# Kernel tuning notes

Measured on AMD Instinct MI355X. Metric: run time of the kernel, lower is better.

The kernel has to match this reference:

```python
import jax, jax.numpy as jnp
import numpy as np
from jax import lax

# db2 (Daubechies-2) filter bank, identical to pywt.Wavelet('db2')
_s3 = np.sqrt(3.0)
_dn = 4.0 * np.sqrt(2.0)
_h = np.array([(1 + _s3) / _dn, (3 + _s3) / _dn, (3 - _s3) / _dn, (1 - _s3) / _dn], dtype=np.float32)  # h0..h3
DEC_LO = jnp.asarray(_h[::-1].copy())                                                # [h3,h2,h1,h0]
DEC_HI = jnp.asarray(np.array([-_h[0], _h[1], -_h[2], _h[3]], dtype=np.float32))
REC_LO = jnp.asarray(_h)                                                             # [h0,h1,h2,h3]
REC_HI = jnp.asarray(np.array([_h[3], -_h[2], _h[1], -_h[0]], dtype=np.float32))
FL = 4  # filter length


def dwt1_symmetric(x):
    """pywt.wavedec level-1, mode='symmetric' along axis 1. x: [B,S,H] -> (cA,cD) each [B,(S+3)//2,H]."""
    B, S, H = x.shape
    M = (S + FL - 1) // 2
    xe = jnp.pad(x, ((0, 0), (FL - 1, FL - 1), (0, 0)), mode='symmetric')  # [B,S+6,H]

    def corr(w):
        # a[k] = sum_t w[FL-1-t] * xe[2k+1+t]
        return sum(w[FL - 1 - t] * xe[:, 1 + t:1 + t + 2 * M:2, :] for t in range(FL))

    return corr(DEC_LO), corr(DEC_HI)


def idwt1(ca, cd):
    """pywt.waverec level-1 (idwt). ca,cd: [B,Mc,H] -> [B,2*Mc-FL+2,H]."""
    B, Mc, H = ca.shape
    up_len = 2 * Mc - 1
    out_len = 2 * Mc - FL + 2

    def branch(c, f):
        u = jnp.zeros((B, up_len + 4, H), dtype=c.dtype)  # zero pad FL-2=2 each side
        u = u.at[:, 2:2 + up_len:2, :].set(c)             # upsample (zeros at odd positions)
        return sum(f[j] * u[:, 4 - j:4 - j + out_len, :] for j in range(FL))

    return branch(ca, REC_LO) + branch(cd, REC_HI)


def conv3_same(c, w, b):
    """torch Conv1d(H,H,3,padding=1) on channel-last c: [B,T,H]; w: [Hout,Hin,3], b: [Hout]."""
    y = lax.conv_general_dilated(c.transpose(0, 2, 1), w, window_strides=(1,),
                                 padding=((1, 1),), dimension_numbers=('NCH', 'OIH', 'NCH'))
    return (y + b[None, :, None]).transpose(0, 2, 1)


def setup_inputs() -> dict:
    key = jax.random.key(0)
    ks = jax.random.split(key, 7)
    B, S, H = 8, 2048, 1024
    sc_conv = 1.0 / np.sqrt(3 * H)
    sc_lin = 1.0 / np.sqrt(H)
    return {
        'x': jax.random.normal(ks[0], (B, S, H), jnp.float32),
        'w_approx': jax.random.normal(ks[1], (H, H, 3), jnp.float32) * sc_conv,
        'b_approx': jax.random.normal(ks[2], (H,), jnp.float32) * 0.01,
        'w_detail': jax.random.normal(ks[3], (H, H, 3), jnp.float32) * sc_conv,
        'b_detail': jax.random.normal(ks[4], (H,), jnp.float32) * 0.01,
        'w_out': jax.random.normal(ks[5], (H, H), jnp.float32) * sc_lin,
        'b_out': jax.random.normal(ks[6], (H,), jnp.float32) * 0.01,
    }


def reference(x, w_approx, b_approx, w_detail, b_detail, w_out, b_out):
    B, S, H = x.shape
    if S % 2 != 0:  # static pad to even length (matches torch code)
        x = jnp.pad(x, ((0, 0), (0, 1), (0, 0)))
        S += 1
    ca, cd = dwt1_symmetric(x)          # [B, S//2+1, H]
    target = S // 2
    ca, cd = ca[:, :target, :], cd[:, :target, :]  # truncate like the torch module
    pa = jax.nn.gelu(conv3_same(ca, w_approx, b_approx), approximate=False)
    pd = jax.nn.gelu(conv3_same(cd, w_detail, b_detail), approximate=False)
    recon = idwt1(pa, pd)               # [B, S-2, H]
    recon = jnp.pad(recon, ((0, 0), (0, S - recon.shape[1]), (0, 0)))  # zero-pad to S
    out = jnp.einsum('bsh,oh->bso', recon, w_out) + b_out  # output_proj; dropout=identity (eval)
    return out
```

## Files before the change

kernel.cpp:

```cpp
#include <hip/hip_runtime.h>
#include <hip/hip_bf16.h>
#include <math.h>


namespace {

constexpr int Hc = 1024;
constexpr int Sc = 2048;
constexpr int Mcv = 1024;
constexpr int AROWS = 1026;

constexpr double S3d = 1.7320508075688772935274463;
constexpr double DNd = 5.6568542494923801952067549;
constexpr float W0 = (float)((1.0 + S3d) / DNd);
constexpr float W1 = (float)((3.0 + S3d) / DNd);
constexpr float W2 = (float)((3.0 - S3d) / DNd);
constexpr float W3 = (float)((1.0 - S3d) / DNd);

typedef short bf16x8 __attribute__((ext_vector_type(8)));
typedef float f32x4 __attribute__((ext_vector_type(4)));

typedef __attribute__((address_space(1))) const unsigned char ga_u8;
typedef __attribute__((address_space(3))) unsigned char la_u8;

__device__ __forceinline__ void gload16(const void* g, void* l) {
  __builtin_amdgcn_global_load_lds((ga_u8*)g, (la_u8*)l, 16, 0, 0);
}

__device__ __forceinline__ unsigned short rnd1(float v) {
  __hip_bfloat16 hb = __float2bfloat16(v);
  return *reinterpret_cast<unsigned short*>(&hb);
}

__device__ __forceinline__ ushort4 rnd4(const float4 v) {
  ushort4 h;
  h.x = rnd1(v.x); h.y = rnd1(v.y); h.z = rnd1(v.z); h.w = rnd1(v.w);
  return h;
}

__device__ __forceinline__ void split1(float v, unsigned short& h, unsigned short& l) {
  __hip_bfloat16 hb = __float2bfloat16(v);
  float r = v - __bfloat162float(hb);
  __hip_bfloat16 lb = __float2bfloat16(r);
  h = *reinterpret_cast<unsigned short*>(&hb);
  l = *reinterpret_cast<unsigned short*>(&lb);
}

__device__ __forceinline__ void split4(const float4 v, ushort4& h, ushort4& l) {
  split1(v.x, h.x, l.x);
  split1(v.y, h.y, l.y);
  split1(v.z, h.z, l.z);
  split1(v.w, h.w, l.w);
}

__global__ void dwt_kernel(const float* __restrict__ x,
                           unsigned short* __restrict__ A) {
  const int tid = blockIdx.x * 256 + threadIdx.x;
  const int h4 = (tid & 255) << 2;
  const int m = (tid >> 8) & (Mcv - 1);
  const int b = tid >> 18;
  const float* xb = x + (size_t)b * Sc * Hc;
  float4 v[4];
#pragma unroll
  for (int t = 0; t < 4; ++t) {
    int i = 2 * m - 2 + t;
    if (i < 0) i = -i - 1;
    v[t] = *reinterpret_cast<const float4*>(&xb[(size_t)i * Hc + h4]);
  }
  float4 a, d;
  a.x = W0 * v[0].x + W1 * v[1].x + W2 * v[2].x + W3 * v[3].x;
  a.y = W0 * v[0].y + W1 * v[1].y + W2 * v[2].y + W3 * v[3].y;
  a.z = W0 * v[0].z + W1 * v[1].z + W2 * v[2].z + W3 * v[3].z;
  a.w = W0 * v[0].w + W1 * v[1].w + W2 * v[2].w + W3 * v[3].w;
  d.x = W3 * v[0].x - W2 * v[1].x + W1 * v[2].x - W0 * v[3].x;
  d.y = W3 * v[0].y - W2 * v[1].y + W1 * v[2].y - W0 * v[3].y;
  d.z = W3 * v[0].z - W2 * v[1].z + W1 * v[2].z - W0 * v[3].z;
  d.w = W3 * v[0].w - W2 * v[1].w + W1 * v[2].w - W0 * v[3].w;

  const size_t rowA = (size_t)b * AROWS + 1 + m;
  const size_t rowD = (size_t)(b + 8) * AROWS + 1 + m;
  *reinterpret_cast<ushort4*>(&A[rowA * Hc + h4]) = rnd4(a);
  *reinterpret_cast<ushort4*>(&A[rowD * Hc + h4]) = rnd4(d);

  if (m == 0) {
    const ushort4 z4 = {0, 0, 0, 0};
    const size_t gr[4] = {(size_t)b * AROWS,       (size_t)b * AROWS + AROWS - 1,
                          (size_t)(b + 8) * AROWS, (size_t)(b + 8) * AROWS + AROWS - 1};
#pragma unroll
    for (int i = 0; i < 4; ++i)
      *reinterpret_cast<ushort4*>(&A[gr[i] * Hc + h4]) = z4;
  }
}

__global__ void prep_conv_w(const float* __restrict__ wA, const float* __restrict__ wD,
                            unsigned short* __restrict__ aH, unsigned short* __restrict__ aL,
                            unsigned short* __restrict__ dH, unsigned short* __restrict__ dL) {
  const int idx = blockIdx.x * 256 + threadIdx.x;
  const int i4 = idx & 255;
  const int o = (idx >> 8) & 1023;
  const int c = idx >> 18;
  const float* w = c ? wD : wA;
  unsigned short* oh = c ? dH : aH;
  unsigned short* ol = c ? dL : aL;
  const float* src = w + (size_t)o * 3072 + i4 * 12;
  const float4 f0 = *reinterpret_cast<const float4*>(src);
  const float4 f1 = *reinterpret_cast<const float4*>(src + 4);
  const float4 f2 = *reinterpret_cast<const float4*>(src + 8);
  const float e[12] = {f0.x, f0.y, f0.z, f0.w, f1.x, f1.y, f1.z, f1.w,
                       f2.x, f2.y, f2.z, f2.w};
#pragma unroll
  for (int k = 0; k < 3; ++k) {
    float4 v = make_float4(e[k], e[3 + k], e[6 + k], e[9 + k]);
    ushort4 hh, ll;
    split4(v, hh, ll);
    const size_t off = (size_t)k * 1048576 + (size_t)o * 1024 + i4 * 4;
    *reinterpret_cast<ushort4*>(&oh[off]) = hh;
    *reinterpret_cast<ushort4*>(&ol[off]) = ll;
  }
}

__global__ void prep_wout(const float* __restrict__ w,
                          unsigned short* __restrict__ oh, unsigned short* __restrict__ ol) {
  const int idx = blockIdx.x * 256 + threadIdx.x;
  const size_t off = (size_t)(idx >> 8) * 1024 + (idx & 255) * 4;
  ushort4 hh, ll;
  split4(*reinterpret_cast<const float4*>(&w[off]), hh, ll);
  *reinterpret_cast<ushort4*>(&oh[off]) = hh;
  *reinterpret_cast<ushort4*>(&ol[off]) = ll;
}

__global__ __launch_bounds__(256, 2) void conv_mm_kernel(
    const unsigned short* __restrict__ A,
    const unsigned short* __restrict__ BAh, const unsigned short* __restrict__ BAl,
    const unsigned short* __restrict__ BDh, const unsigned short* __restrict__ BDl,
    const float* __restrict__ biasA, const float* __restrict__ biasD,
    float* __restrict__ Yout) {
  __shared__ __align__(16) unsigned short lds[32832];

  const int tid = threadIdx.x;
  const int lane = tid & 63;
  const int wave = tid >> 6;
  const int wm = wave >> 1, wn = wave & 1;

  const int id = blockIdx.x;
  const int t = id & 3;
  const int o = (id >> 2) & 7;
  const int z = id >> 5;
  const int o0 = o * 128;
  const int t0 = t * 256;
  const int arow0 = z * AROWS + t0;

  const unsigned short* BH = (z < 8) ? BAh : BDh;
  const unsigned short* BL = (z < 8) ? BAl : BDl;
  const float* bias = (z < 8) ? biasA : biasD;

  f32x4 acc[8][4];
#pragma unroll
  for (int m = 0; m < 8; ++m)
#pragma unroll
    for (int n = 0; n < 4; ++n) acc[m][n] = (f32x4){0.f, 0.f, 0.f, 0.f};

  const int q = lane >> 2;
  const int srcslot = (lane & 3) ^ ((lane >> 3) & 3);
  const int l15 = lane & 15;
  const int g = lane >> 4;

#pragma unroll 1
  for (int c0 = 0; c0 < 1024; c0 += 32) {
    __syncthreads();
#pragma unroll
    for (int j = 0; j < 4; ++j) {
      const int seg = wave * 4 + j;
      const int r = seg * 16 + q;
      gload16(A + (size_t)(arow0 + r) * 1024 + c0 + srcslot * 8, lds + seg * 512);
    }
    if (wave == 0 && lane < 8) {
      const int r = 256 + (lane >> 2);
      gload16(A + (size_t)(arow0 + r) * 1024 + c0 + (lane & 3) * 8, lds + 8192);
    }
#pragma unroll
    for (int tp = 0; tp < 6; ++tp) {
      const unsigned short* bp =
          ((tp & 1) ? BL : BH) + (size_t)(tp >> 1) * 1048576;
      unsigned short* bdst = lds + 8256 + tp * 4096;
#pragma unroll
      for (int j = 0; j < 2; ++j) {
        const int seg = wave * 2 + j;
        const int r = seg * 16 + q;
        gload16(bp + (size_t)(o0 + r) * 1024 + c0 + srcslot * 8, bdst + seg * 512);
      }
    }
    __syncthreads();

#pragma unroll
    for (int tap = 0; tap < 3; ++tap) {
      bf16x8 a4[8], bH4[4], bL4[4];
#pragma unroll
      for (int m = 0; m < 8; ++m) {
        const int r = wm * 128 + m * 16 + l15 + tap;
        const int off = r * 32 + (g ^ ((r >> 1) & 3)) * 8;
        a4[m] = *reinterpret_cast<const bf16x8*>(lds + off);
      }
#pragma unroll
      for (int n = 0; n < 4; ++n) {
        const int r = wn * 64 + n * 16 + l15;
        const int off = r * 32 + (g ^ ((r >> 1) & 3)) * 8;
        bH4[n] = *reinterpret_cast<const bf16x8*>(lds + 8256 + (tap * 2) * 4096 + off);
        bL4[n] = *reinterpret_cast<const bf16x8*>(lds + 8256 + (tap * 2 + 1) * 4096 + off);
      }
#pragma unroll
      for (int m = 0; m < 8; ++m)
#pragma unroll
        for (int n = 0; n < 4; ++n) {
          acc[m][n] = __builtin_amdgcn_mfma_f32_16x16x32_bf16(a4[m], bH4[n], acc[m][n], 0, 0, 0);
          acc[m][n] = __builtin_amdgcn_mfma_f32_16x16x32_bf16(a4[m], bL4[n], acc[m][n], 0, 0, 0);
        }
    }
  }

  const int yrow0 = z * Mcv + t0 + wm * 128;
  constexpr float RS2 = 0.70710678118654752440f;
#pragma unroll
  for (int n = 0; n < 4; ++n) {
    const int col = o0 + wn * 64 + n * 16 + l15;
    const float bv = bias[col];
#pragma unroll
    for (int m = 0; m < 8; ++m) {
      const int rbase = yrow0 + m * 16 + g * 4;
#pragma unroll
      for (int r = 0; r < 4; ++r) {
        float v = acc[m][n][r] + bv;
        v = 0.5f * v * (1.f + erff(v * RS2));
        Yout[(size_t)(rbase + r) * 1024 + col] = v;
      }
    }
  }
}

__global__ void idwt_kernel(const float* __restrict__ pout,
                            unsigned short* __restrict__ rc) {
  const int tid = blockIdx.x * 256 + threadIdx.x;
  const int h4 = (tid & 255) << 2;
  const int s = (tid >> 8) & (Sc - 1);
  const int b = tid >> 19;
  const size_t ro = ((size_t)b * Sc + s) * Hc + h4;
  if (s >= Sc - 2) {
    const ushort4 z4 = {0, 0, 0, 0};
    *reinterpret_cast<ushort4*>(&rc[ro]) = z4;
    return;
  }
  const float* pab = pout + (size_t)b * Mcv * Hc;
  const float* pdb = pout + (size_t)(b + 8) * Mcv * Hc;
  float4 r;
  if ((s & 1) == 0) {
    const int m0 = s >> 1;
    const float4 aL = *reinterpret_cast<const float4*>(&pab[(size_t)m0 * Hc + h4]);
    const float4 aH = *reinterpret_cast<const float4*>(&pab[(size_t)(m0 + 1) * Hc + h4]);
    const float4 dL = *reinterpret_cast<const float4*>(&pdb[(size_t)m0 * Hc + h4]);
    const float4 dH = *reinterpret_cast<const float4*>(&pdb[(size_t)(m0 + 1) * Hc + h4]);
    r.x = W0 * aH.x + W2 * aL.x + W3 * dH.x + W1 * dL.x;
    r.y = W0 * aH.y + W2 * aL.y + W3 * dH.y + W1 * dL.y;
    r.z = W0 * aH.z + W2 * aL.z + W3 * dH.z + W1 * dL.z;
    r.w = W0 * aH.w + W2 * aL.w + W3 * dH.w + W1 * dL.w;
  } else {
    const int ml = (s - 1) >> 1;
    const int mh = ml + 1;
    const float4 aL = *reinterpret_cast<const float4*>(&pab[(size_t)ml * Hc + h4]);
    const float4 aH = *reinterpret_cast<const float4*>(&pab[(size_t)mh * Hc + h4]);
    const float4 dL = *reinterpret_cast<const float4*>(&pdb[(size_t)ml * Hc + h4]);
    const float4 dH = *reinterpret_cast<const float4*>(&pdb[(size_t)mh * Hc + h4]);
    r.x = W1 * aH.x + W3 * aL.x - W2 * dH.x - W0 * dL.x;
    r.y = W1 * aH.y + W3 * aL.y - W2 * dH.y - W0 * dL.y;
    r.z = W1 * aH.z + W3 * aL.z - W2 * dH.z - W0 * dL.z;
    r.w = W1 * aH.w + W3 * aL.w - W2 * dH.w - W0 * dL.w;
  }
  *reinterpret_cast<ushort4*>(&rc[ro]) = rnd4(r);
}

__global__ __launch_bounds__(256, 2) void gemm_out_kernel(
    const unsigned short* __restrict__ Arc,
    const unsigned short* __restrict__ Bhi, const unsigned short* __restrict__ Blo,
    const float* __restrict__ bias, float* __restrict__ out) {
  __shared__ __align__(16) unsigned short lds[16384];
  unsigned short* As = lds;
  unsigned short* BsH = lds + 8192;
  unsigned short* BsL = lds + 12288;

  const int tid = threadIdx.x;
  const int lane = tid & 63;
  const int wave = tid >> 6;
  const int wm = wave >> 1, wn = wave & 1;

  const int id = blockIdx.x;
  const int rowt = (id >> 6) * 8 + (id & 7);
  const int col = (id >> 3) & 7;
  const int o0 = col * 128;
  const int t0 = rowt * 256;

  f32x4 acc[8][4];
#pragma unroll
  for (int m = 0; m < 8; ++m)
#pragma unroll
    for (int n = 0; n < 4; ++n) acc[m][n] = (f32x4){0.f, 0.f, 0.f, 0.f};

  const int q = lane >> 2;
  const int srcslot = (lane & 3) ^ ((lane >> 3) & 3);
  const int l15 = lane & 15;
  const int g = lane >> 4;

#pragma unroll 1
  for (int c0 = 0; c0 < 1024; c0 += 32) {
    __syncthreads();
#pragma unroll
    for (int j = 0; j < 4; ++j) {
      const int seg = wave * 4 + j;
      const int r = seg * 16 + q;
      gload16(Arc + (size_t)(t0 + r) * 1024 + c0 + srcslot * 8, As + seg * 512);
    }
#pragma unroll
    for (int j = 0; j < 2; ++j) {
      const int seg = wave * 2 + j;
      const int r = seg * 16 + q;
      const size_t bsrc = (size_t)(o0 + r) * 1024 + c0 + srcslot * 8;
      gload16(Bhi + bsrc, BsH + seg * 512);
      gload16(Blo + bsrc, BsL + seg * 512);
    }
    __syncthreads();

    bf16x8 a4[8], bH4[4], bL4[4];
#pragma unroll
    for (int m = 0; m < 8; ++m) {
      const int r = wm * 128 + m * 16 + l15;
      const int off = r * 32 + (g ^ ((r >> 1) & 3)) * 8;
      a4[m] = *reinterpret_cast<const bf16x8*>(As + off);
    }
#pragma unroll
    for (int n = 0; n < 4; ++n) {
      const int r = wn * 64 + n * 16 + l15;
      const int off = r * 32 + (g ^ ((r >> 1) & 3)) * 8;
      bH4[n] = *reinterpret_cast<const bf16x8*>(BsH + off);
      bL4[n] = *reinterpret_cast<const bf16x8*>(BsL + off);
    }
#pragma unroll
    for (int m = 0; m < 8; ++m)
#pragma unroll
      for (int n = 0; n < 4; ++n) {
        acc[m][n] = __builtin_amdgcn_mfma_f32_16x16x32_bf16(a4[m], bH4[n], acc[m][n], 0, 0, 0);
        acc[m][n] = __builtin_amdgcn_mfma_f32_16x16x32_bf16(a4[m], bL4[n], acc[m][n], 0, 0, 0);
      }
  }

  const int yrow0 = t0 + wm * 128;
#pragma unroll
  for (int n = 0; n < 4; ++n) {
    const int colg = o0 + wn * 64 + n * 16 + l15;
    const float bv = bias[colg];
#pragma unroll
    for (int m = 0; m < 8; ++m) {
      const int rbase = yrow0 + m * 16 + g * 4;
#pragma unroll
      for (int r = 0; r < 4; ++r)
        out[(size_t)(rbase + r) * 1024 + colg] = acc[m][n][r] + bv;
    }
  }
}

}

extern "C" void kernel_launch(void* const* d_in, const int* in_sizes, int n_in,
                              void* d_out, int out_size, void* d_ws, size_t ws_size,
                              hipStream_t stream) {
  const float* x = (const float*)d_in[0];
  const float* w_approx = (const float*)d_in[1];
  const float* b_approx = (const float*)d_in[2];
  const float* w_detail = (const float*)d_in[3];
  const float* b_detail = (const float*)d_in[4];
  const float* w_out = (const float*)d_in[5];
  const float* b_out = (const float*)d_in[6];
  float* out = (float*)d_out;

  char* ws = (char*)d_ws;
  unsigned short* A = (unsigned short*)(ws);
  float* pout = (float*)(ws + 33619968);
  unsigned short* rc = (unsigned short*)(ws + 100728832);
  unsigned short* wtAh = (unsigned short*)(ws + 134348800);
  unsigned short* wtAl = (unsigned short*)(ws + 140640256);
  unsigned short* wtDh = (unsigned short*)(ws + 146931712);
  unsigned short* wtDl = (unsigned short*)(ws + 153223168);
  unsigned short* woH = (unsigned short*)(ws + 159514624);
  unsigned short* woL = (unsigned short*)(ws + 161611776);

  prep_conv_w<<<2048, 256, 0, stream>>>(w_approx, w_detail, wtAh, wtAl, wtDh, wtDl);
  prep_wout<<<1024, 256, 0, stream>>>(w_out, woH, woL);
  dwt_kernel<<<8192, 256, 0, stream>>>(x, A);

  conv_mm_kernel<<<512, 256, 0, stream>>>(A, wtAh, wtAl, wtDh, wtDl,
                                          b_approx, b_detail, pout);

  idwt_kernel<<<16384, 256, 0, stream>>>(pout, rc);

  gemm_out_kernel<<<512, 256, 0, stream>>>(rc, woH, woL, b_out, out);
}
```

Measured before the change: 432.5 us.

## Double-buffer LDS in conv and output GEMMs, widen conv blocks, pair rows in DWT/IDWT

Both MFMA GEMM kernels now double-buffer their LDS tiles, issuing the loads for the next K-slice before computing the current one, so global loads overlap compute and one barrier per step is dropped. The conv GEMM moves to 512-thread blocks with 8 waves, each covering a 128x32 output sub-tile, and its LDS doubles to about 128KB per block. The DWT and IDWT kernels each now produce two output rows per thread, reusing the overlapping input rows and halving the grid. The larger LDS use and 512-thread blocks may lower occupancy, and the extra buffer loads add register pressure.

```diff
diff --git a/kernel.cpp b/kernel.cpp
--- a/kernel.cpp
+++ b/kernel.cpp
@@ -57,32 +57,39 @@
                            unsigned short* __restrict__ A) {
   const int tid = blockIdx.x * 256 + threadIdx.x;
   const int h4 = (tid & 255) << 2;
-  const int m = (tid >> 8) & (Mcv - 1);
-  const int b = tid >> 18;
+  const int mp = (tid >> 8) & 511;
+  const int b = tid >> 17;
+  const int m = mp * 2;
   const float* xb = x + (size_t)b * Sc * Hc;
-  float4 v[4];
-#pragma unroll
-  for (int t = 0; t < 4; ++t) {
+  float4 v[6];
+#pragma unroll
+  for (int t = 0; t < 6; ++t) {
     int i = 2 * m - 2 + t;
     if (i < 0) i = -i - 1;
     v[t] = *reinterpret_cast<const float4*>(&xb[(size_t)i * Hc + h4]);
   }
-  float4 a, d;
-  a.x = W0 * v[0].x + W1 * v[1].x + W2 * v[2].x + W3 * v[3].x;
-  a.y = W0 * v[0].y + W1 * v[1].y + W2 * v[2].y + W3 * v[3].y;
-  a.z = W0 * v[0].z + W1 * v[1].z + W2 * v[2].z + W3 * v[3].z;
-  a.w = W0 * v[0].w + W1 * v[1].w + W2 * v[2].w + W3 * v[3].w;
-  d.x = W3 * v[0].x - W2 * v[1].x + W1 * v[2].x - W0 * v[3].x;
-  d.y = W3 * v[0].y - W2 * v[1].y + W1 * v[2].y - W0 * v[3].y;
-  d.z = W3 * v[0].z - W2 * v[1].z + W1 * v[2].z - W0 * v[3].z;
-  d.w = W3 * v[0].w - W2 * v[1].w + W1 * v[2].w - W0 * v[3].w;
+  float4 a0, d0, a1, d1;
+#define DWT_AD(ao, dd, u0, u1, u2, u3)                      \
+  ao.x = W0*u0.x + W1*u1.x + W2*u2.x + W3*u3.x;             \
+  ao.y = W0*u0.y + W1*u1.y + W2*u2.y + W3*u3.y;             \
+  ao.z = W0*u0.z + W1*u1.z + W2*u2.z + W3*u3.z;             \
+  ao.w = W0*u0.w + W1*u1.w + W2*u2.w + W3*u3.w;             \
+  dd.x = W3*u0.x - W2*u1.x + W1*u2.x - W0*u3.x;             \
+  dd.y = W3*u0.y - W2*u1.y + W1*u2.y - W0*u3.y;             \
+  dd.z = W3*u0.z - W2*u1.z + W1*u2.z - W0*u3.z;             \
+  dd.w = W3*u0.w - W2*u1.w + W1*u2.w - W0*u3.w;
+  DWT_AD(a0, d0, v[0], v[1], v[2], v[3]);
+  DWT_AD(a1, d1, v[2], v[3], v[4], v[5]);
+#undef DWT_AD
 
   const size_t rowA = (size_t)b * AROWS + 1 + m;
   const size_t rowD = (size_t)(b + 8) * AROWS + 1 + m;
-  *reinterpret_cast<ushort4*>(&A[rowA * Hc + h4]) = rnd4(a);
-  *reinterpret_cast<ushort4*>(&A[rowD * Hc + h4]) = rnd4(d);
-
-  if (m == 0) {
+  *reinterpret_cast<ushort4*>(&A[rowA * Hc + h4]) = rnd4(a0);
+  *reinterpret_cast<ushort4*>(&A[(rowA + 1) * Hc + h4]) = rnd4(a1);
+  *reinterpret_cast<ushort4*>(&A[rowD * Hc + h4]) = rnd4(d0);
+  *reinterpret_cast<ushort4*>(&A[(rowD + 1) * Hc + h4]) = rnd4(d1);
+
+  if (mp == 0) {
     const ushort4 z4 = {0, 0, 0, 0};
     const size_t gr[4] = {(size_t)b * AROWS,       (size_t)b * AROWS + AROWS - 1,
                           (size_t)(b + 8) * AROWS, (size_t)(b + 8) * AROWS + AROWS - 1};
@@ -129,18 +136,19 @@
   *reinterpret_cast<ushort4*>(&ol[off]) = ll;
 }
 
-__global__ __launch_bounds__(256, 2) void conv_mm_kernel(
+__global__ __launch_bounds__(512, 2) void conv_mm_kernel(
     const unsigned short* __restrict__ A,
     const unsigned short* __restrict__ BAh, const unsigned short* __restrict__ BAl,
     const unsigned short* __restrict__ BDh, const unsigned short* __restrict__ BDl,
     const float* __restrict__ biasA, const float* __restrict__ biasD,
     float* __restrict__ Yout) {
-  __shared__ __align__(16) unsigned short lds[32832];
+  __shared__ __align__(16) unsigned short lds[65664];
 
   const int tid = threadIdx.x;
   const int lane = tid & 63;
   const int wave = tid >> 6;
-  const int wm = wave >> 1, wn = wave & 1;
+  const int wm = wave >> 2;
+  const int wn = wave & 3;
 
   const int id = blockIdx.x;
   const int t = id & 3;
@@ -154,75 +162,85 @@
   const unsigned short* BL = (z < 8) ? BAl : BDl;
   const float* bias = (z < 8) ? biasA : biasD;
 
-  f32x4 acc[8][4];
+  f32x4 acc[8][2];
 #pragma unroll
   for (int m = 0; m < 8; ++m)
 #pragma unroll
-    for (int n = 0; n < 4; ++n) acc[m][n] = (f32x4){0.f, 0.f, 0.f, 0.f};
+    for (int n = 0; n < 2; ++n) acc[m][n] = (f32x4){0.f, 0.f, 0.f, 0.f};
 
   const int q = lane >> 2;
   const int srcslot = (lane & 3) ^ ((lane >> 3) & 3);
   const int l15 = lane & 15;
   const int g = lane >> 4;
 
+#define CONV_STAGE(buf, c0)                                                     \
+  {                                                                             \
+    unsigned short* L = lds + (buf) * 32832;                                    \
+    _Pragma("unroll")                                                           \
+    for (int j = 0; j < 2; ++j) {                                               \
+      const int seg = wave * 2 + j;                                             \
+      const int r = seg * 16 + q;                                               \
+      gload16(A + (size_t)(arow0 + r) * 1024 + (c0) + srcslot * 8,              \
+              L + seg * 512);                                                   \
+    }                                                                           \
+    if (wave == 0 && lane < 8) {                                                \
+      const int r = 256 + (lane >> 2);                                          \
+      gload16(A + (size_t)(arow0 + r) * 1024 + (c0) + (lane & 3) * 8,           \
+              L + 8192);                                                        \
+    }                                                                           \
+    _Pragma("unroll")                                                           \
+    for (int j = 0; j < 6; ++j) {                                               \
+      const int g6 = wave * 6 + j;                                              \
+      const int tp = g6 >> 3;                                                   \
+      const int seg = g6 & 7;                                                   \
+      const unsigned short* bp =                                                \
+          ((tp & 1) ? BL : BH) + (size_t)(tp >> 1) * 1048576;                   \
+      const int r = seg * 16 + q;                                               \
+      gload16(bp + (size_t)(o0 + r) * 1024 + (c0) + srcslot * 8,                \
+              L + 8256 + tp * 4096 + seg * 512);                                \
+    }                                                                           \
+  }
+
+  CONV_STAGE(0, 0);
+  __syncthreads();
+
+  int cur = 0;
 #pragma unroll 1
-  for (int c0 = 0; c0 < 1024; c0 += 32) {
-    __syncthreads();
-#pragma unroll
-    for (int j = 0; j < 4; ++j) {
-      const int seg = wave * 4 + j;
-      const int r = seg * 16 + q;
-      gload16(A + (size_t)(arow0 + r) * 1024 + c0 + srcslot * 8, lds + seg * 512);
-    }
-    if (wave == 0 && lane < 8) {
-      const int r = 256 + (lane >> 2);
-      gload16(A + (size_t)(arow0 + r) * 1024 + c0 + (lane & 3) * 8, lds + 8192);
-    }
-#pragma unroll
-    for (int tp = 0; tp < 6; ++tp) {
-      const unsigned short* bp =
-          ((tp & 1) ? BL : BH) + (size_t)(tp >> 1) * 1048576;
-      unsigned short* bdst = lds + 8256 + tp * 4096;
-#pragma unroll
-      for (int j = 0; j < 2; ++j) {
-        const int seg = wave * 2 + j;
-        const int r = seg * 16 + q;
-        gload16(bp + (size_t)(o0 + r) * 1024 + c0 + srcslot * 8, bdst + seg * 512);
+  for (int step = 0; step < 32; ++step) {
+    if (step < 31) CONV_STAGE(cur ^ 1, (step + 1) * 32);
+
+    unsigned short* L = lds + cur * 32832;
+#pragma unroll
+    for (int tap = 0; tap < 3; ++tap) {
+      bf16x8 a4[8];
+#pragma unroll
+      for (int m = 0; m < 8; ++m) {
+        const int r = wm * 128 + m * 16 + l15 + tap;
+        a4[m] = *reinterpret_cast<const bf16x8*>(L + r * 32 + (g ^ ((r >> 1) & 3)) * 8);
+      }
+#pragma unroll
+      for (int n = 0; n < 2; ++n) {
+        const int r = wn * 32 + n * 16 + l15;
+        const int off = r * 32 + (g ^ ((r >> 1) & 3)) * 8;
+        const bf16x8 bH4 = *reinterpret_cast<const bf16x8*>(L + 8256 + (tap * 2) * 4096 + off);
+        const bf16x8 bL4 = *reinterpret_cast<const bf16x8*>(L + 8256 + (tap * 2 + 1) * 4096 + off);
+#pragma unroll
+        for (int m = 0; m < 8; ++m) {
+          acc[m][n] = __builtin_amdgcn_mfma_f32_16x16x32_bf16(a4[m], bH4, acc[m][n], 0, 0, 0);
+          acc[m][n] = __builtin_amdgcn_mfma_f32_16x16x32_bf16(a4[m], bL4, acc[m][n], 0, 0, 0);
+        }
       }
     }
     __syncthreads();
-
-#pragma unroll
-    for (int tap = 0; tap < 3; ++tap) {
-      bf16x8 a4[8], bH4[4], bL4[4];
-#pragma unroll
-      for (int m = 0; m < 8; ++m) {
-        const int r = wm * 128 + m * 16 + l15 + tap;
-        const int off = r * 32 + (g ^ ((r >> 1) & 3)) * 8;
-        a4[m] = *reinterpret_cast<const bf16x8*>(lds + off);
-      }
-#pragma unroll
-      for (int n = 0; n < 4; ++n) {
-        const int r = wn * 64 + n * 16 + l15;
-        const int off = r * 32 + (g ^ ((r >> 1) & 3)) * 8;
-        bH4[n] = *reinterpret_cast<const bf16x8*>(lds + 8256 + (tap * 2) * 4096 + off);
-        bL4[n] = *reinterpret_cast<const bf16x8*>(lds + 8256 + (tap * 2 + 1) * 4096 + off);
-      }
-#pragma unroll
-      for (int m = 0; m < 8; ++m)
-#pragma unroll
-        for (int n = 0; n < 4; ++n) {
-          acc[m][n] = __builtin_amdgcn_mfma_f32_16x16x32_bf16(a4[m], bH4[n], acc[m][n], 0, 0, 0);
-          acc[m][n] = __builtin_amdgcn_mfma_f32_16x16x32_bf16(a4[m], bL4[n], acc[m][n], 0, 0, 0);
-        }
-    }
-  }
+    cur ^= 1;
+  }
+#undef CONV_STAGE
 
   const int yrow0 = z * Mcv + t0 + wm * 128;
   constexpr float RS2 = 0.70710678118654752440f;
 #pragma unroll
-  for (int n = 0; n < 4; ++n) {
-    const int col = o0 + wn * 64 + n * 16 + l15;
+  for (int n = 0; n < 2; ++n) {
+    const int col = o0 + wn * 32 + n * 16 + l15;
     const float bv = bias[col];
 #pragma unroll
     for (int m = 0; m < 8; ++m) {
@@ -241,50 +259,39 @@
                             unsigned short* __restrict__ rc) {
   const int tid = blockIdx.x * 256 + threadIdx.x;
   const int h4 = (tid & 255) << 2;
-  const int s = (tid >> 8) & (Sc - 1);
-  const int b = tid >> 19;
-  const size_t ro = ((size_t)b * Sc + s) * Hc + h4;
-  if (s >= Sc - 2) {
+  const int j = (tid >> 8) & 1023;
+  const int b = tid >> 18;
+  const size_t ro = ((size_t)b * Sc + 2 * j) * Hc + h4;
+  if (j == 1023) {
     const ushort4 z4 = {0, 0, 0, 0};
     *reinterpret_cast<ushort4*>(&rc[ro]) = z4;
+    *reinterpret_cast<ushort4*>(&rc[ro + Hc]) = z4;
     return;
   }
   const float* pab = pout + (size_t)b * Mcv * Hc;
   const float* pdb = pout + (size_t)(b + 8) * Mcv * Hc;
-  float4 r;
-  if ((s & 1) == 0) {
-    const int m0 = s >> 1;
-    const float4 aL = *reinterpret_cast<const float4*>(&pab[(size_t)m0 * Hc + h4]);
-    const float4 aH = *reinterpret_cast<const float4*>(&pab[(size_t)(m0 + 1) * Hc + h4]);
-    const float4 dL = *reinterpret_cast<const float4*>(&pdb[(size_t)m0 * Hc + h4]);
-    const float4 dH = *reinterpret_cast<const float4*>(&pdb[(size_t)(m0 + 1) * Hc + h4]);
-    r.x = W0 * aH.x + W2 * aL.x + W3 * dH.x + W1 * dL.x;
-    r.y = W0 * aH.y + W2 * aL.y + W3 * dH.y + W1 * dL.y;
-    r.z = W0 * aH.z + W2 * aL.z + W3 * dH.z + W1 * dL.z;
-    r.w = W0 * aH.w + W2 * aL.w + W3 * dH.w + W1 * dL.w;
-  } else {
-    const int ml = (s - 1) >> 1;
-    const int mh = ml + 1;
-    const float4 aL = *reinterpret_cast<const float4*>(&pab[(size_t)ml * Hc + h4]);
-    const float4 aH = *reinterpret_cast<const float4*>(&pab[(size_t)mh * Hc + h4]);
-    const float4 dL = *reinterpret_cast<const float4*>(&pdb[(size_t)ml * Hc + h4]);
-    const float4 dH = *reinterpret_cast<const float4*>(&pdb[(size_t)mh * Hc + h4]);
-    r.x = W1 * aH.x + W3 * aL.x - W2 * dH.x - W0 * dL.x;
-    r.y = W1 * aH.y + W3 * aL.y - W2 * dH.y - W0 * dL.y;
-    r.z = W1 * aH.z + W3 * aL.z - W2 * dH.z - W0 * dL.z;
-    r.w = W1 * aH.w + W3 * aL.w - W2 * dH.w - W0 * dL.w;
-  }
-  *reinterpret_cast<ushort4*>(&rc[ro]) = rnd4(r);
+  const float4 aL = *reinterpret_cast<const float4*>(&pab[(size_t)j * Hc + h4]);
+  const float4 aH = *reinterpret_cast<const float4*>(&pab[(size_t)(j + 1) * Hc + h4]);
+  const float4 dL = *reinterpret_cast<const float4*>(&pdb[(size_t)j * Hc + h4]);
+  const float4 dH = *reinterpret_cast<const float4*>(&pdb[(size_t)(j + 1) * Hc + h4]);
+  float4 r0, r1;
+  r0.x = W0 * aH.x + W2 * aL.x + W3 * dH.x + W1 * dL.x;
+  r0.y = W0 * aH.y + W2 * aL.y + W3 * dH.y + W1 * dL.y;
+  r0.z = W0 * aH.z + W2 * aL.z + W3 * dH.z + W1 * dL.z;
+  r0.w = W0 * aH.w + W2 * aL.w + W3 * dH.w + W1 * dL.w;
+  r1.x = W1 * aH.x + W3 * aL.x - W2 * dH.x - W0 * dL.x;
+  r1.y = W1 * aH.y + W3 * aL.y - W2 * dH.y - W0 * dL.y;
+  r1.z = W1 * aH.z + W3 * aL.z - W2 * dH.z - W0 * dL.z;
+  r1.w = W1 * aH.w + W3 * aL.w - W2 * dH.w - W0 * dL.w;
+  *reinterpret_cast<ushort4*>(&rc[ro]) = rnd4(r0);
+  *reinterpret_cast<ushort4*>(&rc[ro + Hc]) = rnd4(r1);
 }
 
 __global__ __launch_bounds__(256, 2) void gemm_out_kernel(
     const unsigned short* __restrict__ Arc,
     const unsigned short* __restrict__ Bhi, const unsigned short* __restrict__ Blo,
     const float* __restrict__ bias, float* __restrict__ out) {
-  __shared__ __align__(16) unsigned short lds[16384];
-  unsigned short* As = lds;
-  unsigned short* BsH = lds + 8192;
-  unsigned short* BsL = lds + 12288;
+  __shared__ __align__(16) unsigned short lds[32768];
 
   const int tid = threadIdx.x;
   const int lane = tid & 63;
@@ -308,38 +315,49 @@
   const int l15 = lane & 15;
   const int g = lane >> 4;
 
+#define GEMM_STAGE(buf, c0)                                                     \
+  {                                                                             \
+    unsigned short* L = lds + (buf) * 16384;                                    \
+    _Pragma("unroll")                                                           \
+    for (int j = 0; j < 4; ++j) {                                               \
+      const int seg = wave * 4 + j;                                             \
+      const int r = seg * 16 + q;                                               \
+      gload16(Arc + (size_t)(t0 + r) * 1024 + (c0) + srcslot * 8,               \
+              L + seg * 512);                                                   \
+    }                                                                           \
+    _Pragma("unroll")                                                           \
+    for (int j = 0; j < 4; ++j) {                                               \
+      const int g4 = wave * 4 + j;                                              \
+      const int pl = g4 >> 3;                                                   \
+      const int seg = g4 & 7;                                                   \
+      const unsigned short* bp = pl ? Blo : Bhi;                                \
+      const int r = seg * 16 + q;                                               \
+      gload16(bp + (size_t)(o0 + r) * 1024 + (c0) + srcslot * 8,                \
+              L + 8192 + pl * 4096 + seg * 512);                                \
+    }                                                                           \
+  }
+
+  GEMM_STAGE(0, 0);
+  __syncthreads();
+
+  int cur = 0;
 #pragma unroll 1
-  for (int c0 = 0; c0 < 1024; c0 += 32) {
-    __syncthreads();
-#pragma unroll
-    for (int j = 0; j < 4; ++j) {
-      const int seg = wave * 4 + j;
-      const int r = seg * 16 + q;
-      gload16(Arc + (size_t)(t0 + r) * 1024 + c0 + srcslot * 8, As + seg * 512);
-    }
-#pragma unroll
-    for (int j = 0; j < 2; ++j) {
-      const int seg = wave * 2 + j;
-      const int r = seg * 16 + q;
-      const size_t bsrc = (size_t)(o0 + r) * 1024 + c0 + srcslot * 8;
-      gload16(Bhi + bsrc, BsH + seg * 512);
-      gload16(Blo + bsrc, BsL + seg * 512);
-    }
-    __syncthreads();
-
+  for (int step = 0; step < 32; ++step) {
+    if (step < 31) GEMM_STAGE(cur ^ 1, (step + 1) * 32);
+
+    unsigned short* L = lds + cur * 16384;
     bf16x8 a4[8], bH4[4], bL4[4];
 #pragma unroll
     for (int m = 0; m < 8; ++m) {
       const int r = wm * 128 + m * 16 + l15;
-      const int off = r * 32 + (g ^ ((r >> 1) & 3)) * 8;
-      a4[m] = *reinterpret_cast<const bf16x8*>(As + off);
+      a4[m] = *reinterpret_cast<const bf16x8*>(L + r * 32 + (g ^ ((r >> 1) & 3)) * 8);
     }
 #pragma unroll
     for (int n = 0; n < 4; ++n) {
       const int r = wn * 64 + n * 16 + l15;
       const int off = r * 32 + (g ^ ((r >> 1) & 3)) * 8;
-      bH4[n] = *reinterpret_cast<const bf16x8*>(BsH + off);
-      bL4[n] = *reinterpret_cast<const bf16x8*>(BsL + off);
+      bH4[n] = *reinterpret_cast<const bf16x8*>(L + 8192 + off);
+      bL4[n] = *reinterpret_cast<const bf16x8*>(L + 12288 + off);
     }
 #pragma unroll
     for (int m = 0; m < 8; ++m)
@@ -348,7 +366,10 @@
         acc[m][n] = __builtin_amdgcn_mfma_f32_16x16x32_bf16(a4[m], bH4[n], acc[m][n], 0, 0, 0);
         acc[m][n] = __builtin_amdgcn_mfma_f32_16x16x32_bf16(a4[m], bL4[n], acc[m][n], 0, 0, 0);
       }
-  }
+    __syncthreads();
+    cur ^= 1;
+  }
+#undef GEMM_STAGE
 
   const int yrow0 = t0 + wm * 128;
 #pragma unroll
@@ -392,12 +413,12 @@
 
   prep_conv_w<<<2048, 256, 0, stream>>>(w_approx, w_detail, wtAh, wtAl, wtDh, wtDl);
   prep_wout<<<1024, 256, 0, stream>>>(w_out, woH, woL);
-  dwt_kernel<<<8192, 256, 0, stream>>>(x, A);
-
-  conv_mm_kernel<<<512, 256, 0, stream>>>(A, wtAh, wtAl, wtDh, wtDl,
+  dwt_kernel<<<4096, 256, 0, stream>>>(x, A);
+
+  conv_mm_kernel<<<512, 512, 0, stream>>>(A, wtAh, wtAl, wtDh, wtDl,
                                           b_approx, b_detail, pout);
 
-  idwt_kernel<<<16384, 256, 0, stream>>>(pout, rc);
+  idwt_kernel<<<8192, 256, 0, stream>>>(pout, rc);
 
   gemm_out_kernel<<<512, 256, 0, stream>>>(rc, woH, woL, b_out, out);
 }
```

New measurement: 408.9 us. -5.5%, faster.
